# Optimization experiments

Measured on AMD Instinct MI355X. Metric: run time of the kernel, lower is better.

## Reference

```python
import jax, jax.numpy as jnp
import numpy as np
import math

H = 512      # d_model
N = 64       # d_state
B = 16
L = 4096
DT_MIN, DT_MAX = 0.001, 0.1


def setup_inputs() -> dict:
    key = jax.random.key(0)
    ks = jax.random.split(key, 6)
    u = jax.random.normal(ks[0], (B, H, L), dtype=jnp.float32)
    # S4DKernel parameters
    C = jax.random.normal(ks[1], (H, N // 2, 2), dtype=jnp.float32)  # view_as_real of cfloat C
    log_dt = (jax.random.uniform(ks[2], (H,), dtype=jnp.float32)
              * (math.log(DT_MAX) - math.log(DT_MIN)) + math.log(DT_MIN))
    log_A_real = jnp.log(0.5 * jnp.ones((H, N // 2), dtype=jnp.float32))
    A_imag = math.pi * jnp.broadcast_to(jnp.arange(N // 2, dtype=jnp.float32), (H, N // 2))
    # S4D parameters
    D = jax.random.normal(ks[3], (H,), dtype=jnp.float32)
    # output_linear: Conv1d(H, 2H, kernel_size=1) -> weight (2H, H), bias (2H,)
    W = jax.random.normal(ks[4], (2 * H, H), dtype=jnp.float32) * (1.0 / math.sqrt(H))
    b = jax.random.normal(ks[5], (2 * H,), dtype=jnp.float32) * 0.01
    return {"u": u, "C": C, "log_dt": log_dt, "log_A_real": log_A_real,
            "A_imag": A_imag, "D": D, "W": W, "b": b}


def _s4d_kernel(C, log_dt, log_A_real, A_imag, L):
    """Generate the (H, L) convolution kernel from diagonal SSM parameters."""
    dt = jnp.exp(log_dt)                                    # (H,)
    Cc = C[..., 0] + 1j * C[..., 1]                         # (H, N/2) complex
    A = -jnp.exp(log_A_real) + 1j * A_imag                  # (H, N/2)
    dtA = A * dt[:, None]                                   # (H, N/2)
    # Vandermonde: exp(dtA * l) for l in [0, L)
    K = jnp.exp(dtA[:, :, None] * jnp.arange(L, dtype=jnp.float32))  # (H, N/2, L)
    Cw = Cc * (jnp.exp(dtA) - 1.0) / A                      # (H, N/2)
    k = 2.0 * jnp.einsum('hn,hnl->hl', Cw, K).real          # (H, L)
    return k


def reference(u, C, log_dt, log_A_real, A_imag, D, W, b):
    Lc = u.shape[-1]
    k = _s4d_kernel(C, log_dt, log_A_real, A_imag, Lc)      # (H, L)
    # FFT long convolution (linear conv via zero-padding to 2L)
    k_f = jnp.fft.rfft(k, n=2 * Lc)                          # (H, L+1)
    u_f = jnp.fft.rfft(u, n=2 * Lc)                          # (B, H, L+1)
    y = jnp.fft.irfft(u_f * k_f, n=2 * Lc)[..., :Lc]         # (B, H, L)
    y = y + u * D[:, None]
    y = jax.nn.gelu(y, approximate=False)                    # torch nn.GELU default
    # output_linear: 1x1 Conv1d (H -> 2H) then GLU over channel dim
    z = jnp.einsum('oh,bhl->bol', W, y) + b[None, :, None]   # (B, 2H, L)
    a, g = jnp.split(z, 2, axis=1)
    return a * jax.nn.sigmoid(g)                             # (B, H, L)
```

## Files before the change

kernel.cpp:

```cpp
#include <hip/hip_runtime.h>

#define BB 16
#define HH 512
#define NH 32
#define LL 4096
#define TCH 64
#define NCH 64
#define KA 128

static_assert(TCH * NCH == LL, "chunking");

typedef __attribute__((ext_vector_type(8))) short bf16x8;
typedef __attribute__((ext_vector_type(4))) float f32x4;

static __device__ __forceinline__ unsigned short f2bf(float x) {
    return __builtin_bit_cast(unsigned short, (__bf16)x);
}
static __device__ __forceinline__ float bf2f(unsigned short b) {
    return __builtin_bit_cast(float, ((unsigned)b) << 16);
}
static __device__ __forceinline__ unsigned pack2(float a, float b) {
    return (unsigned)f2bf(a) | ((unsigned)f2bf(b) << 16);
}
static __device__ __forceinline__ float gelu1(float x) {
    float a = fmaf(0.071354816f * x, x * x, 1.5957691f * x);
    return x * __builtin_amdgcn_rcpf(1.0f + __expf(-a));
}

static __device__ __forceinline__ void gload_lds16(const void* g, void* l) {
#if __has_builtin(__builtin_amdgcn_global_load_lds)
    __builtin_amdgcn_global_load_lds(
        (const __attribute__((address_space(1))) unsigned int*)g,
        (__attribute__((address_space(3))) unsigned int*)l, 16, 0, 0);
#else
    *(uint4*)l = *(const uint4*)g;
#endif
}

__global__ void k0_params(const float* __restrict__ C,
                          const float* __restrict__ log_dt,
                          const float* __restrict__ lAr,
                          const float* __restrict__ Aim,
                          float* __restrict__ c2R,  float* __restrict__ c2I,
                          float* __restrict__ ltR,  float* __restrict__ ltI,
                          float* __restrict__ xrA,  float* __restrict__ xiA)
{
    int tid = blockIdx.x * 256 + threadIdx.x;
    if (tid >= HH * NH) return;
    int h = tid >> 5;
    float dt = expf(log_dt[h]);
    float Ar = -expf(lAr[tid]);
    float Ai = Aim[tid];
    float xr = Ar * dt, xi = Ai * dt;
    xrA[tid] = xr; xiA[tid] = xi;
    float er = expf(xr);
    float lr = er * cosf(xi);
    float li = er * sinf(xi);
    float wr = lr - 1.0f, wi = li;
    float inv = 1.0f / (Ar * Ar + Ai * Ai);
    float qr = (wr * Ar + wi * Ai) * inv;
    float qi = (wi * Ar - wr * Ai) * inv;
    float cr = C[2 * tid], ci = C[2 * tid + 1];
    c2R[tid] =  2.0f * (cr * qr - ci * qi);
    c2I[tid] = -2.0f * (cr * qi + ci * qr);
    float eT = expf((float)TCH * xr);
    float aT = (float)TCH * xi;
    ltR[tid] = eT * cosf(aT);
    ltI[tid] = eT * sinf(aT);
}

__global__ void kw_pack(const float* __restrict__ W, const float* __restrict__ bias,
                        unsigned short* __restrict__ Wp, float* __restrict__ bp)
{
    int tid = blockIdx.x * 256 + threadIdx.x;
    int drow = tid >> 6;
    int kc = (tid & 63) * 8;
    int src = (drow & 1) ? (drow >> 1) + HH : (drow >> 1);
    const float4* s = (const float4*)(W + (size_t)src * HH + kc);
    float4 a = s[0], b4 = s[1];
    uint4 pack;
    pack.x = pack2(a.x, a.y);
    pack.y = pack2(a.z, a.w);
    pack.z = pack2(b4.x, b4.y);
    pack.w = pack2(b4.z, b4.w);
    *(uint4*)(Wp + (size_t)drow * HH + kc) = pack;
    if (tid < 2 * HH)
        bp[tid] = bias[(tid & 1) ? (tid >> 1) + HH : (tid >> 1)];
}

__global__ __launch_bounds__(64) void kA_build(
    const float* __restrict__ c2R, const float* __restrict__ c2I,
    const float* __restrict__ xrA, const float* __restrict__ xiA,
    const float* __restrict__ Dv,
    unsigned short* __restrict__ Apan, unsigned short* __restrict__ Vpan)
{
    int h = blockIdx.x;
    int t = threadIdx.x;
    __shared__ float s_xr[NH], s_xi[NH], s_cr[NH], s_ci[NH], s_k[TCH];
    if (t < NH) {
        s_xr[t] = xrA[h * NH + t]; s_xi[t] = xiA[h * NH + t];
        s_cr[t] = c2R[h * NH + t]; s_ci[t] = c2I[h * NH + t];
    }
    __syncthreads();
    {
        float d = (float)t;
        float acc = 0.f;
#pragma unroll
        for (int n = 0; n < NH; ++n) {
            float er = __expf(s_xr[n] * d);
            float sv, cv; __sincosf(s_xi[n] * d, &sv, &cv);
            acc = fmaf(s_cr[n], er * cv, fmaf(s_ci[n], er * sv, acc));
        }
        s_k[t] = acc;
    }
    __syncthreads();
    float k0d = s_k[0] + Dv[h];
    unsigned short row[KA];
#pragma unroll
    for (int tau = 0; tau < TCH; ++tau)
        row[tau] = f2bf((tau < t) ? s_k[t - tau] : (tau == t ? k0d : 0.f));
    float tp = (float)(t + 1);
#pragma unroll
    for (int n = 0; n < NH; ++n) {
        float er = __expf(s_xr[n] * tp);
        float sv, cv; __sincosf(s_xi[n] * tp, &sv, &cv);
        float pr = er * cv, pi = er * sv;
        row[TCH + 2 * n]     = f2bf(fmaf(s_cr[n], pr,  s_ci[n] * pi));
        row[TCH + 2 * n + 1] = f2bf(fmaf(s_ci[n], pr, -s_cr[n] * pi));
    }
    {
        uint4* dst = (uint4*)(Apan + ((size_t)h * TCH + t) * KA);
        const uint4* src = (const uint4*)row;
#pragma unroll
        for (int i = 0; i < 16; ++i) dst[i] = src[i];
    }
    {
        int n = t >> 1, cm = t & 1;
        float xr = s_xr[n], xi = s_xi[n];
        unsigned short vrow[TCH];
#pragma unroll
        for (int tau = 0; tau < TCH; ++tau) {
            float p = (float)(TCH - 1 - tau);
            float er = __expf(xr * p);
            float sv, cv; __sincosf(xi * p, &sv, &cv);
            vrow[tau] = f2bf(cm ? er * sv : er * cv);
        }
        uint4* vd = (uint4*)(Vpan + ((size_t)h * TCH + t) * TCH);
        const uint4* vs = (const uint4*)vrow;
#pragma unroll
        for (int i = 0; i < 8; ++i) vd[i] = vs[i];
    }
}

__global__ __launch_bounds__(256)
__attribute__((amdgpu_waves_per_eu(2)))
void kBCD(
    const float* __restrict__ u,
    const unsigned short* __restrict__ Apan, const unsigned short* __restrict__ Vpan,
    const float* __restrict__ ltR, const float* __restrict__ ltI,
    unsigned short* __restrict__ yb)
{
    __shared__ unsigned short Sl[4][TCH * TCH];
    int h = blockIdx.x & (HH - 1), g = blockIdx.x >> 9;
    int tid = threadIdx.x;
    int lane = tid & 63, w = tid >> 6;
    int b = g * 4 + w;
    int lrow = lane & 15, hi = lane >> 4, lk8 = hi * 8;
    const float* ug = u + ((size_t)b * HH + h) * LL;
    const unsigned short* Ap = Apan + (size_t)h * TCH * KA;
    const unsigned short* Vp = Vpan + (size_t)h * TCH * TCH;
    char* Sw = (char*)Sl[w];

    bf16x8 ub[2][4];
#pragma unroll
    for (int ks = 0; ks < 2; ++ks)
#pragma unroll
        for (int n = 0; n < 4; ++n) {
            int c = n * 16 + lrow;
            const float* up = ug + c * TCH + ks * 32 + lk8;
            float4 f0 = *(const float4*)up, f1 = *(const float4*)(up + 4);
            bf16x8 v;
            v[0]=f2bf(f0.x); v[1]=f2bf(f0.y); v[2]=f2bf(f0.z); v[3]=f2bf(f0.w);
            v[4]=f2bf(f1.x); v[5]=f2bf(f1.y); v[6]=f2bf(f1.z); v[7]=f2bf(f1.w);
            ub[ks][n] = v;
        }

#pragma unroll
    for (int m = 0; m < 4; ++m) {
        f32x4 accE[4];
#pragma unroll
        for (int n = 0; n < 4; ++n) { f32x4 z = {0.f,0.f,0.f,0.f}; accE[n] = z; }
#pragma unroll
        for (int ks = 0; ks < 2; ++ks) {
            bf16x8 vf = *(const bf16x8*)(Vp + (m * 16 + lrow) * TCH + ks * 32 + lk8);
#pragma unroll
            for (int n = 0; n < 4; ++n)
                accE[n] = __builtin_amdgcn_mfma_f32_16x16x32_bf16(vf, ub[ks][n], accE[n], 0, 0, 0);
        }
        int j0 = m * 16 + hi * 4;
#pragma unroll
        for (int n = 0; n < 4; ++n) {
            int c = n * 16 + lrow;
            uint2 p; p.x = pack2(accE[n][0], accE[n][1]); p.y = pack2(accE[n][2], accE[n][3]);
            *(uint2*)(Sw + c * 128 + ((2 * j0) ^ ((c & 7) << 4))) = p;
        }
    }
    asm volatile("s_waitcnt lgkmcnt(0)" ::: "memory");

    if (lane < NH) {
        int n = lane;
        float ar = ltR[h * NH + n], ai = ltI[h * NH + n];
        float sr = 0.f, si = 0.f;
#pragma unroll
        for (int gg = 0; gg < 8; ++gg) {
            unsigned ev[8];
#pragma unroll
            for (int k = 0; k < 8; ++k)
                ev[k] = *(const unsigned*)(Sw + (gg * 8 + k) * 128 + ((4 * n) ^ (k << 4)));
#pragma unroll
            for (int k = 0; k < 8; ++k) {
                *(unsigned*)(Sw + (gg * 8 + k) * 128 + ((4 * n) ^ (k << 4))) = pack2(sr, si);
                float er = bf2f((unsigned short)(ev[k] & 0xffffu));
                float ei = bf2f((unsigned short)(ev[k] >> 16));
                float nsr = fmaf(ar, sr, fmaf(-ai, si, er));
                float nsi = fmaf(ar, si, fmaf(ai, sr, ei));
                sr = nsr; si = nsi;
            }
        }
    }
    asm volatile("s_waitcnt lgkmcnt(0)" ::: "memory");

    bf16x8 sfr[2][4];
#pragma unroll
    for (int ks = 0; ks < 2; ++ks)
#pragma unroll
        for (int n = 0; n < 4; ++n) {
            int c = n * 16 + lrow;
            sfr[ks][n] = *(const bf16x8*)(Sw + c * 128 + ((ks * 64 + lk8 * 2) ^ ((c & 7) << 4)));
        }

    uint2 yp[4][4];
#pragma unroll
    for (int m = 0; m < 4; ++m) {
        f32x4 acc[4];
#pragma unroll
        for (int n = 0; n < 4; ++n) { f32x4 z = {0.f,0.f,0.f,0.f}; acc[n] = z; }
#pragma unroll
        for (int ks = 0; ks < 2; ++ks) {
            bf16x8 af = *(const bf16x8*)(Ap + (m * 16 + lrow) * KA + ks * 32 + lk8);
#pragma unroll
            for (int n = 0; n < 4; ++n)
                acc[n] = __builtin_amdgcn_mfma_f32_16x16x32_bf16(af, ub[ks][n], acc[n], 0, 0, 0);
        }
#pragma unroll
        for (int ks = 0; ks < 2; ++ks) {
            bf16x8 af = *(const bf16x8*)(Ap + (m * 16 + lrow) * KA + 64 + ks * 32 + lk8);
#pragma unroll
            for (int n = 0; n < 4; ++n)
                acc[n] = __builtin_amdgcn_mfma_f32_16x16x32_bf16(af, sfr[ks][n], acc[n], 0, 0, 0);
        }
#pragma unroll
        for (int n = 0; n < 4; ++n) {
            yp[m][n].x = pack2(gelu1(acc[n][0]), gelu1(acc[n][1]));
            yp[m][n].y = pack2(gelu1(acc[n][2]), gelu1(acc[n][3]));
        }
    }
    asm volatile("s_waitcnt lgkmcnt(0)" ::: "memory");

#pragma unroll
    for (int m = 0; m < 4; ++m) {
        int t0b = m * 32 + hi * 8;
#pragma unroll
        for (int n = 0; n < 4; ++n) {
            int c = n * 16 + lrow;
            *(uint2*)(Sw + c * 128 + (t0b ^ ((c & 7) << 4))) = yp[m][n];
        }
    }
    asm volatile("s_waitcnt lgkmcnt(0)" ::: "memory");
    unsigned short* yrow = yb + ((size_t)b * HH + h) * LL;
#pragma unroll
    for (int it = 0; it < 8; ++it) {
        int o = it * 1024 + lane * 16;
        int c = o >> 7;
        int sl = o & 127;
        uint4 v = *(const uint4*)(Sw + c * 128 + (sl ^ ((c & 7) << 4)));
        *(uint4*)((char*)yrow + o) = v;
    }
}

__global__ __launch_bounds__(256) void kT_transpose(
    const unsigned short* __restrict__ yb, unsigned short* __restrict__ yt)
{
    __shared__ unsigned short T[64][130];
    int bid = blockIdx.x;
    int lt = bid & 31;
    int ht = (bid >> 5) & 7;
    int b  = bid >> 8;
    int t = threadIdx.x;
#pragma unroll
    for (int r = 0; r < 4; ++r) {
        int chunk = r * 256 + t;
        int row = chunk >> 4;
        int c16 = chunk & 15;
        uint4 v = *(const uint4*)(yb + ((size_t)(b * HH + ht * 64 + row)) * LL
                                     + lt * 128 + c16 * 8);
        *(uint4*)&T[row][c16 * 8] = v;
    }
    __syncthreads();
    int oct = t & 7, lgrp = t >> 3;
    size_t obase = ((size_t)b * LL + (size_t)lt * 128) * HH + ht * 64 + oct * 8;
#pragma unroll
    for (int r = 0; r < 2; ++r) {
        int l = (r * 32 + lgrp) * 2;
        unsigned v[8];
#pragma unroll
        for (int k = 0; k < 8; ++k)
            v[k] = *(const unsigned*)&T[oct * 8 + k][l];
        uint4 w0, w1;
        w0.x = (v[0] & 0xffffu) | (v[1] << 16);
        w0.y = (v[2] & 0xffffu) | (v[3] << 16);
        w0.z = (v[4] & 0xffffu) | (v[5] << 16);
        w0.w = (v[6] & 0xffffu) | (v[7] << 16);
        w1.x = (v[0] >> 16) | (v[1] & 0xffff0000u);
        w1.y = (v[2] >> 16) | (v[3] & 0xffff0000u);
        w1.z = (v[4] >> 16) | (v[5] & 0xffff0000u);
        w1.w = (v[6] >> 16) | (v[7] & 0xffff0000u);
        *(uint4*)(yt + obase + (size_t)l * HH) = w0;
        *(uint4*)(yt + obase + (size_t)(l + 1) * HH) = w1;
    }
}

#define BM 128
#define BN 128
#define BKK 32
#define NKT (HH / BKK)

__global__ __launch_bounds__(256, 4) void k4_gemm(
    const unsigned short* __restrict__ Wp, const float* __restrict__ bp,
    const unsigned short* __restrict__ yt, float* __restrict__ out)
{
    __shared__ unsigned short As[2][BM * BKK];
    __shared__ unsigned short Bs[2][BN * BKK];
    int tid  = threadIdx.x;
    int bidx = (blockIdx.x & 7) * 512 + (blockIdx.x >> 3);
    int mtile = bidx & 7, ntile = bidx >> 3;
    int mbase = mtile * BM, nbase = ntile * BN;
    int lane = tid & 63;
    int wv = tid >> 6;
    int wr = wv >> 1, wc = wv & 1;
    int lrow = lane & 15;
    int hi = lane >> 4;

    int srow0 = tid >> 2, sc16 = tid & 3;
    int skc0 = (sc16 ^ ((srow0 >> 1) & 3)) * 8;
    int srow1 = (256 + tid) >> 2;
    int skc1 = (sc16 ^ ((srow1 >> 1) & 3)) * 8;
    const unsigned short* aAddr0 = Wp + (size_t)(mbase + srow0) * HH + skc0;
    const unsigned short* bAddr0 = yt + (size_t)(nbase + srow0) * HH + skc0;
    const unsigned short* aAddr1 = Wp + (size_t)(mbase + srow1) * HH + skc1;
    const unsigned short* bAddr1 = yt + (size_t)(nbase + srow1) * HH + skc1;

    f32x4 acc[4][4];
#pragma unroll
    for (int m = 0; m < 4; ++m)
#pragma unroll
        for (int n = 0; n < 4; ++n) { f32x4 z = {0.f,0.f,0.f,0.f}; acc[m][n] = z; }

    gload_lds16(aAddr0, &As[0][tid * 8]);
    gload_lds16(bAddr0, &Bs[0][tid * 8]);
    gload_lds16(aAddr1, &As[0][(256 + tid) * 8]);
    gload_lds16(bAddr1, &Bs[0][(256 + tid) * 8]);
    __syncthreads();

    for (int t = 0; t < NKT; ++t) {
        int cur = t & 1;
        if (t + 1 < NKT) {
            int kk = (t + 1) * BKK;
            gload_lds16(aAddr0 + kk, &As[cur ^ 1][tid * 8]);
            gload_lds16(bAddr0 + kk, &Bs[cur ^ 1][tid * 8]);
            gload_lds16(aAddr1 + kk, &As[cur ^ 1][(256 + tid) * 8]);
            gload_lds16(bAddr1 + kk, &Bs[cur ^ 1][(256 + tid) * 8]);
        }
        bf16x8 af[4], bfr[4];
#pragma unroll
        for (int m = 0; m < 4; ++m) {
            int row = wr * 64 + m * 16 + lrow;
            int slot = hi ^ ((row >> 1) & 3);
            af[m] = *(const bf16x8*)&As[cur][row * BKK + slot * 8];
        }
#pragma unroll
        for (int nf = 0; nf < 4; ++nf) {
            int row = wc * 64 + nf * 16 + lrow;
            int slot = hi ^ ((row >> 1) & 3);
            bfr[nf] = *(const bf16x8*)&Bs[cur][row * BKK + slot * 8];
        }
#pragma unroll
        for (int m = 0; m < 4; ++m)
#pragma unroll
            for (int nf = 0; nf < 4; ++nf)
                acc[m][nf] = __builtin_amdgcn_mfma_f32_16x16x32_bf16(af[m], bfr[nf], acc[m][nf], 0, 0, 0);
        __syncthreads();
    }
#pragma unroll
    for (int m = 0; m < 4; ++m) {
        int go = mbase + wr * 64 + m * 16 + (hi * 4);
        float4 bv = *(const float4*)(bp + go);
#pragma unroll
        for (int nf = 0; nf < 4; ++nf) {
            int col  = nbase + wc * 64 + nf * 16 + lrow;
            int bcol = col >> 12;
            int lcol = col & (LL - 1);
            f32x4 v = acc[m][nf];
            float a0 = v[0] + bv.x, g0 = v[1] + bv.y;
            float a1 = v[2] + bv.z, g1 = v[3] + bv.w;
            float o0 = a0 / (1.0f + __expf(-g0));
            float o1 = a1 / (1.0f + __expf(-g1));
            size_t ob = ((size_t)bcol * HH + (size_t)(go >> 1)) * LL + lcol;
            out[ob] = o0;
            out[ob + LL] = o1;
        }
    }
}

extern "C" void kernel_launch(void* const* d_in, const int* in_sizes, int n_in,
                              void* d_out, int out_size, void* d_ws, size_t ws_size,
                              hipStream_t stream) {
    const float* u    = (const float*)d_in[0];
    const float* C    = (const float*)d_in[1];
    const float* ldt  = (const float*)d_in[2];
    const float* lar  = (const float*)d_in[3];
    const float* aim  = (const float*)d_in[4];
    const float* Dv   = (const float*)d_in[5];
    const float* W    = (const float*)d_in[6];
    const float* bias = (const float*)d_in[7];
    float* out = (float*)d_out;

    char* w = (char*)d_ws;
    float* c2R = (float*)w; w += (size_t)HH * NH * 4;
    float* c2I = (float*)w; w += (size_t)HH * NH * 4;
    float* ltR = (float*)w; w += (size_t)HH * NH * 4;
    float* ltI = (float*)w; w += (size_t)HH * NH * 4;
    float* xrA = (float*)w; w += (size_t)HH * NH * 4;
    float* xiA = (float*)w; w += (size_t)HH * NH * 4;
    float* bp  = (float*)w; w += (size_t)2 * HH * 4;
    unsigned short* Wp   = (unsigned short*)w; w += (size_t)2 * HH * HH * 2;
    unsigned short* Apan = (unsigned short*)w; w += (size_t)HH * TCH * KA * 2;
    unsigned short* Vpan = (unsigned short*)w; w += (size_t)HH * TCH * TCH * 2;
    unsigned short* yt   = (unsigned short*)w; w += (size_t)BB * LL * HH * 2;

    unsigned short* yb = (unsigned short*)d_out;

    k0_params   <<<dim3(64),   dim3(256), 0, stream>>>(C, ldt, lar, aim, c2R, c2I, ltR, ltI, xrA, xiA);
    kw_pack     <<<dim3(256),  dim3(256), 0, stream>>>(W, bias, Wp, bp);
    kA_build    <<<dim3(512),  dim3(64),  0, stream>>>(c2R, c2I, xrA, xiA, Dv, Apan, Vpan);
    kBCD        <<<dim3(2048), dim3(256), 0, stream>>>(u, Apan, Vpan, ltR, ltI, yb);
    kT_transpose<<<dim3(4096), dim3(256), 0, stream>>>(yb, yt);
    k4_gemm     <<<dim3(4096), dim3(256), 0, stream>>>(Wp, bp, yt, out);
}
```

Measured before the change: 189.4 us.

## Fuse y transpose into GEMM B-tile loading and drop transpose kernel

Removes the separate transpose kernel that rewrote the bf16 activation tensor from (B,H,L) to (B,L,H) layout. The GEMM now reads the (B,H,L) buffer directly with register loads, transposes pairs of channels in registers, and writes them into the swizzled LDS tile after the MFMA work of each step. This saves a full read and write of the 64 MB intermediate and one launch. In exchange, B tiles use ordinary global loads plus scattered 4-byte LDS stores instead of direct global-to-LDS loads, and each row read is strided by L. yb also moves from the output buffer to the workspace.

```diff
diff --git a/kernel.cpp b/kernel.cpp
--- a/kernel.cpp
+++ b/kernel.cpp
@@ -288,48 +288,6 @@
     }
 }
 
-__global__ __launch_bounds__(256) void kT_transpose(
-    const unsigned short* __restrict__ yb, unsigned short* __restrict__ yt)
-{
-    __shared__ unsigned short T[64][130];
-    int bid = blockIdx.x;
-    int lt = bid & 31;
-    int ht = (bid >> 5) & 7;
-    int b  = bid >> 8;
-    int t = threadIdx.x;
-#pragma unroll
-    for (int r = 0; r < 4; ++r) {
-        int chunk = r * 256 + t;
-        int row = chunk >> 4;
-        int c16 = chunk & 15;
-        uint4 v = *(const uint4*)(yb + ((size_t)(b * HH + ht * 64 + row)) * LL
-                                     + lt * 128 + c16 * 8);
-        *(uint4*)&T[row][c16 * 8] = v;
-    }
-    __syncthreads();
-    int oct = t & 7, lgrp = t >> 3;
-    size_t obase = ((size_t)b * LL + (size_t)lt * 128) * HH + ht * 64 + oct * 8;
-#pragma unroll
-    for (int r = 0; r < 2; ++r) {
-        int l = (r * 32 + lgrp) * 2;
-        unsigned v[8];
-#pragma unroll
-        for (int k = 0; k < 8; ++k)
-            v[k] = *(const unsigned*)&T[oct * 8 + k][l];
-        uint4 w0, w1;
-        w0.x = (v[0] & 0xffffu) | (v[1] << 16);
-        w0.y = (v[2] & 0xffffu) | (v[3] << 16);
-        w0.z = (v[4] & 0xffffu) | (v[5] << 16);
-        w0.w = (v[6] & 0xffffu) | (v[7] << 16);
-        w1.x = (v[0] >> 16) | (v[1] & 0xffff0000u);
-        w1.y = (v[2] >> 16) | (v[3] & 0xffff0000u);
-        w1.z = (v[4] >> 16) | (v[5] & 0xffff0000u);
-        w1.w = (v[6] >> 16) | (v[7] & 0xffff0000u);
-        *(uint4*)(yt + obase + (size_t)l * HH) = w0;
-        *(uint4*)(yt + obase + (size_t)(l + 1) * HH) = w1;
-    }
-}
-
 #define BM 128
 #define BN 128
 #define BKK 32
@@ -337,7 +295,7 @@
 
 __global__ __launch_bounds__(256, 4) void k4_gemm(
     const unsigned short* __restrict__ Wp, const float* __restrict__ bp,
-    const unsigned short* __restrict__ yt, float* __restrict__ out)
+    const unsigned short* __restrict__ yb, float* __restrict__ out)
 {
     __shared__ unsigned short As[2][BM * BKK];
     __shared__ unsigned short Bs[2][BN * BKK];
@@ -353,12 +311,30 @@
 
     int srow0 = tid >> 2, sc16 = tid & 3;
     int skc0 = (sc16 ^ ((srow0 >> 1) & 3)) * 8;
-    int srow1 = (256 + tid) >> 2;
+    int srow1 = 64 + srow0;
     int skc1 = (sc16 ^ ((srow1 >> 1) & 3)) * 8;
     const unsigned short* aAddr0 = Wp + (size_t)(mbase + srow0) * HH + skc0;
-    const unsigned short* bAddr0 = yt + (size_t)(nbase + srow0) * HH + skc0;
     const unsigned short* aAddr1 = Wp + (size_t)(mbase + srow1) * HH + skc1;
-    const unsigned short* bAddr1 = yt + (size_t)(nbase + srow1) * HH + skc1;
+
+    int bb = nbase >> 12;
+    int lbase = nbase & (LL - 1);
+    const unsigned short* ybp = yb + ((size_t)bb * HH) * LL + lbase;
+    int hp = tid & 15;
+    int l0 = (tid >> 4) * 8;
+    const unsigned short* bAddr = ybp + (size_t)(2 * hp) * LL + l0;
+
+#define BWRITE(buf, R0, R1) do {                                               \
+    char* _Bb = (char*)&Bs[buf][0];                                            \
+    _Pragma("unroll")                                                          \
+    for (int _j = 0; _j < 8; ++_j) {                                           \
+        unsigned _wa = ((const unsigned*)&(R0))[_j >> 1];                      \
+        unsigned _wb = ((const unsigned*)&(R1))[_j >> 1];                      \
+        unsigned _sa = (_j & 1) ? (_wa >> 16) : (_wa & 0xffffu);               \
+        unsigned _sb = (_j & 1) ? (_wb >> 16) : (_wb & 0xffffu);               \
+        int _row = l0 + _j;                                                    \
+        int _bo = (((hp >> 2) ^ ((_row >> 1) & 3)) << 4) + ((4 * hp) & 15);    \
+        *(unsigned*)(_Bb + _row * 64 + _bo) = _sa | (_sb << 16);               \
+    } } while (0)
 
     f32x4 acc[4][4];
 #pragma unroll
@@ -367,19 +343,24 @@
         for (int n = 0; n < 4; ++n) { f32x4 z = {0.f,0.f,0.f,0.f}; acc[m][n] = z; }
 
     gload_lds16(aAddr0, &As[0][tid * 8]);
-    gload_lds16(bAddr0, &Bs[0][tid * 8]);
     gload_lds16(aAddr1, &As[0][(256 + tid) * 8]);
-    gload_lds16(bAddr1, &Bs[0][(256 + tid) * 8]);
+    {
+        uint4 r0 = *(const uint4*)bAddr;
+        uint4 r1 = *(const uint4*)(bAddr + LL);
+        BWRITE(0, r0, r1);
+    }
     __syncthreads();
 
     for (int t = 0; t < NKT; ++t) {
         int cur = t & 1;
-        if (t + 1 < NKT) {
+        uint4 n0, n1;
+        bool more = (t + 1 < NKT);
+        if (more) {
             int kk = (t + 1) * BKK;
             gload_lds16(aAddr0 + kk, &As[cur ^ 1][tid * 8]);
-            gload_lds16(bAddr0 + kk, &Bs[cur ^ 1][tid * 8]);
             gload_lds16(aAddr1 + kk, &As[cur ^ 1][(256 + tid) * 8]);
-            gload_lds16(bAddr1 + kk, &Bs[cur ^ 1][(256 + tid) * 8]);
+            n0 = *(const uint4*)(bAddr + (size_t)kk * LL);
+            n1 = *(const uint4*)(bAddr + (size_t)kk * LL + LL);
         }
         bf16x8 af[4], bfr[4];
 #pragma unroll
@@ -399,8 +380,12 @@
 #pragma unroll
             for (int nf = 0; nf < 4; ++nf)
                 acc[m][nf] = __builtin_amdgcn_mfma_f32_16x16x32_bf16(af[m], bfr[nf], acc[m][nf], 0, 0, 0);
+        if (more)
+            BWRITE(cur ^ 1, n0, n1);
         __syncthreads();
     }
+#undef BWRITE
+
 #pragma unroll
     for (int m = 0; m < 4; ++m) {
         int go = mbase + wr * 64 + m * 16 + (hi * 4);
@@ -446,14 +431,11 @@
     unsigned short* Wp   = (unsigned short*)w; w += (size_t)2 * HH * HH * 2;
     unsigned short* Apan = (unsigned short*)w; w += (size_t)HH * TCH * KA * 2;
     unsigned short* Vpan = (unsigned short*)w; w += (size_t)HH * TCH * TCH * 2;
-    unsigned short* yt   = (unsigned short*)w; w += (size_t)BB * LL * HH * 2;
-
-    unsigned short* yb = (unsigned short*)d_out;
-
-    k0_params   <<<dim3(64),   dim3(256), 0, stream>>>(C, ldt, lar, aim, c2R, c2I, ltR, ltI, xrA, xiA);
-    kw_pack     <<<dim3(256),  dim3(256), 0, stream>>>(W, bias, Wp, bp);
-    kA_build    <<<dim3(512),  dim3(64),  0, stream>>>(c2R, c2I, xrA, xiA, Dv, Apan, Vpan);
-    kBCD        <<<dim3(2048), dim3(256), 0, stream>>>(u, Apan, Vpan, ltR, ltI, yb);
-    kT_transpose<<<dim3(4096), dim3(256), 0, stream>>>(yb, yt);
-    k4_gemm     <<<dim3(4096), dim3(256), 0, stream>>>(Wp, bp, yt, out);
-}
+    unsigned short* yb   = (unsigned short*)w; w += (size_t)BB * LL * HH * 2;
+
+    k0_params<<<dim3(64),   dim3(256), 0, stream>>>(C, ldt, lar, aim, c2R, c2I, ltR, ltI, xrA, xiA);
+    kw_pack  <<<dim3(256),  dim3(256), 0, stream>>>(W, bias, Wp, bp);
+    kA_build <<<dim3(512),  dim3(64),  0, stream>>>(c2R, c2I, xrA, xiA, Dv, Apan, Vpan);
+    kBCD     <<<dim3(2048), dim3(256), 0, stream>>>(u, Apan, Vpan, ltR, ltI, yb);
+    k4_gemm  <<<dim3(4096), dim3(256), 0, stream>>>(Wp, bp, yb, out);
+}
```

Result: faster. 182.2 us (-3.8%).
